# Optimization experiments

Hardware: AMD Instinct MI355X
Metric: run time of the kernel (lower is better)

## Reference

```python
import jax, jax.numpy as jnp
import numpy as np

INPUT_DIM = 1024
HIDDEN_DIM = 1024
BATCH = 8
SEQ = 2048


def setup_inputs() -> dict:
    key = jax.random.key(0)
    ks = jax.random.split(key, 7)
    s = 1.0 / np.sqrt(INPUT_DIM)
    return {
        "subgraph_embeddings": jax.random.normal(ks[0], (BATCH, SEQ, INPUT_DIM), dtype=jnp.float32),
        "Wq": jax.random.uniform(ks[1], (INPUT_DIM, HIDDEN_DIM), jnp.float32, -s, s),
        "bq": jax.random.uniform(ks[2], (HIDDEN_DIM,), jnp.float32, -s, s),
        "Wk": jax.random.uniform(ks[3], (INPUT_DIM, HIDDEN_DIM), jnp.float32, -s, s),
        "bk": jax.random.uniform(ks[4], (HIDDEN_DIM,), jnp.float32, -s, s),
        "Wv": jax.random.uniform(ks[5], (INPUT_DIM, HIDDEN_DIM), jnp.float32, -s, s),
        "bv": jax.random.uniform(ks[6], (HIDDEN_DIM,), jnp.float32, -s, s),
    }


def reference(subgraph_embeddings, Wq, bq, Wk, bk, Wv, bv):
    x = subgraph_embeddings  # [B, S, D]
    Q = jnp.einsum('bsd,dh->bsh', x, Wq) + bq
    K = jnp.einsum('bsd,dh->bsh', x, Wk) + bk
    V = jnp.einsum('bsd,dh->bsh', x, Wv) + bv
    scale = jnp.sqrt(jnp.float32(HIDDEN_DIM))
    scores = jnp.einsum('bqh,bkh->bqk', Q, K) / scale  # [B, S, S]
    weights = jax.nn.softmax(scores, axis=-1)
    return jnp.einsum('bqk,bkh->bqh', weights, V)
```

## Files before the change

kernel.cpp:

```cpp
#include <hip/hip_runtime.h>
#include <hip/hip_bf16.h>
#include <stdint.h>

typedef unsigned short u16;
typedef unsigned int u32;
typedef __attribute__((ext_vector_type(8))) short bf16x8;
typedef __attribute__((ext_vector_type(4))) float f32x4;

#define S_LEN 2048
#define D_DIM 1024
#define H_DIM 1024
#define BATCH 8
#define M_TOTAL (BATCH * S_LEN)

__device__ __forceinline__ u16 f2b(float f) {
  u32 u = __builtin_bit_cast(u32, f);
  u32 r = (u + 0x7fffu + ((u >> 16) & 1u)) >> 16;
  return (u16)r;
}
__device__ __forceinline__ float b2f(u16 v) {
  u32 u = ((u32)v) << 16;
  return __builtin_bit_cast(float, u);
}

__global__ __launch_bounds__(256) void cast_x_kernel(const float* __restrict__ in,
                                                     u16* __restrict__ out, int n8) {
  int i = blockIdx.x * 256 + threadIdx.x;
  if (i >= n8) return;
  const float4* p = (const float4*)in;
  float4 a = p[2 * i], b = p[2 * i + 1];
  u32 w0 = (u32)f2b(a.x) | ((u32)f2b(a.y) << 16);
  u32 w1 = (u32)f2b(a.z) | ((u32)f2b(a.w) << 16);
  u32 w2 = (u32)f2b(b.x) | ((u32)f2b(b.y) << 16);
  u32 w3 = (u32)f2b(b.z) | ((u32)f2b(b.w) << 16);
  ((uint4*)out)[i] = make_uint4(w0, w1, w2, w3);
}

__global__ __launch_bounds__(256) void wcast_kernel(const float* __restrict__ W,
                                                    u16* __restrict__ Wt) {
  __shared__ float tile[32][33];
  int h0 = blockIdx.x * 32, d0 = blockIdx.y * 32;
  int tx = threadIdx.x & 31, ty = threadIdx.x >> 5;
#pragma unroll
  for (int r = ty; r < 32; r += 8)
    tile[r][tx] = W[(size_t)(d0 + r) * H_DIM + h0 + tx];
  __syncthreads();
#pragma unroll
  for (int r = ty; r < 32; r += 8)
    Wt[(size_t)(h0 + r) * D_DIM + d0 + tx] = f2b(tile[tx][r]);
}

template <int BIAS_MODE, bool OUT_BF16>
__global__ __launch_bounds__(256) void gemm_bt(const u16* __restrict__ A,
                                               const u16* __restrict__ Bt,
                                               void* __restrict__ Cout,
                                               const float* __restrict__ bias,
                                               int M, int N, int K,
                                               long long aBatch, long long bBatch,
                                               long long cBatch) {
  __shared__ __align__(16) u16 As[128 * 64];
  __shared__ __align__(16) u16 Bs[128 * 64];
  const int tid = threadIdx.x;
  const int wave = tid >> 6, lane = tid & 63;
  const int quad = lane >> 4, lr = lane & 15;
  const int wr = (wave >> 1) * 64, wc = (wave & 1) * 64;
  const int row0 = blockIdx.x * 128, col0 = blockIdx.y * 128;
  A += (size_t)blockIdx.z * (size_t)aBatch;
  Bt += (size_t)blockIdx.z * (size_t)bBatch;

  f32x4 acc[4][4] = {};

  auto AsL = (__attribute__((address_space(3))) char*)As;
  auto BsL = (__attribute__((address_space(3))) char*)Bs;
  const char* Ab = (const char*)A;
  const char* Bb = (const char*)Bt;

  for (int k0 = 0; k0 < K; k0 += 64) {
#pragma unroll
    for (int rr = 0; rr < 4; ++rr) {
      int chunk = rr * 256 + tid;
      int row = chunk >> 3;
      int cs = (chunk & 7) ^ (row & 7);
      const void* ga = Ab + (((size_t)(row0 + row) * K + (size_t)k0 + cs * 8) * 2);
      __builtin_amdgcn_global_load_lds(
          (const __attribute__((address_space(1))) void*)ga,
          (__attribute__((address_space(3))) void*)(AsL + chunk * 16), 16, 0, 0);
      const void* gb = Bb + (((size_t)(col0 + row) * K + (size_t)k0 + cs * 8) * 2);
      __builtin_amdgcn_global_load_lds(
          (const __attribute__((address_space(1))) void*)gb,
          (__attribute__((address_space(3))) void*)(BsL + chunk * 16), 16, 0, 0);
    }
    __syncthreads();
#pragma unroll
    for (int ks = 0; ks < 2; ++ks) {
      bf16x8 af[4], bf[4];
#pragma unroll
      for (int i = 0; i < 4; ++i) {
        int r = wr + i * 16 + lr;
        int cc = (ks * 4 + quad) ^ (r & 7);
        af[i] = *(const bf16x8*)&As[r * 64 + cc * 8];
      }
#pragma unroll
      for (int j = 0; j < 4; ++j) {
        int r = wc + j * 16 + lr;
        int cc = (ks * 4 + quad) ^ (r & 7);
        bf[j] = *(const bf16x8*)&Bs[r * 64 + cc * 8];
      }
#pragma unroll
      for (int i = 0; i < 4; ++i)
#pragma unroll
        for (int j = 0; j < 4; ++j)
          acc[i][j] = __builtin_amdgcn_mfma_f32_16x16x32_bf16(af[i], bf[j],
                                                              acc[i][j], 0, 0, 0);
    }
    __syncthreads();
  }

  if constexpr (OUT_BF16) {
    u16* C = (u16*)Cout + (size_t)blockIdx.z * (size_t)cBatch;
#pragma unroll
    for (int i = 0; i < 4; ++i) {
#pragma unroll
      for (int j = 0; j < 4; ++j) {
        int c = col0 + wc + j * 16 + lr;
        float bcol = (BIAS_MODE == 1) ? bias[c] : 0.f;
#pragma unroll
        for (int ii = 0; ii < 4; ++ii) {
          int r = row0 + wr + i * 16 + quad * 4 + ii;
          float v = acc[i][j][ii] + bcol;
          if (BIAS_MODE == 2) v += bias[r];
          C[(size_t)r * N + c] = f2b(v);
        }
      }
    }
  } else {
    float* C = (float*)Cout + (size_t)blockIdx.z * (size_t)cBatch;
#pragma unroll
    for (int i = 0; i < 4; ++i) {
#pragma unroll
      for (int j = 0; j < 4; ++j) {
        int c = col0 + wc + j * 16 + lr;
        float bcol = (BIAS_MODE == 1) ? bias[c] : 0.f;
#pragma unroll
        for (int ii = 0; ii < 4; ++ii) {
          int r = row0 + wr + i * 16 + quad * 4 + ii;
          float v = acc[i][j][ii] + bcol;
          if (BIAS_MODE == 2) v += bias[r];
          C[(size_t)r * N + c] = v;
        }
      }
    }
  }
}

__global__ __launch_bounds__(256) void softmax_kernel(u16* __restrict__ S, float scale) {
  __shared__ float red[8];
  const int row = blockIdx.x;
  const int tid = threadIdx.x;
  const int wave = tid >> 6, lane = tid & 63;
  u16* rp = S + (size_t)row * S_LEN;
  uint4 q = ((const uint4*)rp)[tid];
  u32 w[4] = {q.x, q.y, q.z, q.w};
  float v[8];
#pragma unroll
  for (int k = 0; k < 4; ++k) {
    v[2 * k] = b2f((u16)(w[k] & 0xffffu)) * scale;
    v[2 * k + 1] = b2f((u16)(w[k] >> 16)) * scale;
  }
  float m = v[0];
#pragma unroll
  for (int k = 1; k < 8; ++k) m = fmaxf(m, v[k]);
#pragma unroll
  for (int off = 32; off > 0; off >>= 1) m = fmaxf(m, __shfl_xor(m, off));
  if (lane == 0) red[wave] = m;
  __syncthreads();
  m = fmaxf(fmaxf(red[0], red[1]), fmaxf(red[2], red[3]));
  float e[8], s = 0.f;
#pragma unroll
  for (int k = 0; k < 8; ++k) {
    e[k] = __expf(v[k] - m);
    s += e[k];
  }
#pragma unroll
  for (int off = 32; off > 0; off >>= 1) s += __shfl_xor(s, off);
  if (lane == 0) red[4 + wave] = s;
  __syncthreads();
  float inv = 1.0f / (red[4] + red[5] + red[6] + red[7]);
  u32 o[4];
#pragma unroll
  for (int k = 0; k < 4; ++k)
    o[k] = (u32)f2b(e[2 * k] * inv) | ((u32)f2b(e[2 * k + 1] * inv) << 16);
  ((uint4*)rp)[tid] = make_uint4(o[0], o[1], o[2], o[3]);
}

extern "C" void kernel_launch(void* const* d_in, const int* in_sizes, int n_in,
                              void* d_out, int out_size, void* d_ws, size_t ws_size,
                              hipStream_t stream) {
  const float* x = (const float*)d_in[0];
  const float* Wq = (const float*)d_in[1];
  const float* bq = (const float*)d_in[2];
  const float* Wk = (const float*)d_in[3];
  const float* bk = (const float*)d_in[4];
  const float* Wv = (const float*)d_in[5];
  const float* bv = (const float*)d_in[6];
  float* out = (float*)d_out;

  char* ws = (char*)d_ws;
  u16* xb = (u16*)ws;  ws += (size_t)M_TOTAL * D_DIM * 2;
  u16* Wtq = (u16*)ws; ws += (size_t)H_DIM * D_DIM * 2;
  u16* Wtk = (u16*)ws; ws += (size_t)H_DIM * D_DIM * 2;
  u16* Wtv = (u16*)ws; ws += (size_t)H_DIM * D_DIM * 2;
  u16* Qm = (u16*)ws;  ws += (size_t)M_TOTAL * H_DIM * 2;
  u16* Km = (u16*)ws;  ws += (size_t)M_TOTAL * H_DIM * 2;
  u16* Vt = (u16*)ws;  ws += (size_t)BATCH * H_DIM * S_LEN * 2;
  u16* Sm = (u16*)ws;  ws += (size_t)BATCH * S_LEN * S_LEN * 2;

  cast_x_kernel<<<(M_TOTAL * D_DIM / 8 + 255) / 256, 256, 0, stream>>>(
      x, xb, M_TOTAL * D_DIM / 8);
  wcast_kernel<<<dim3(32, 32), 256, 0, stream>>>(Wq, Wtq);
  wcast_kernel<<<dim3(32, 32), 256, 0, stream>>>(Wk, Wtk);
  wcast_kernel<<<dim3(32, 32), 256, 0, stream>>>(Wv, Wtv);

  gemm_bt<1, true><<<dim3(128, 8, 1), 256, 0, stream>>>(
      xb, Wtq, Qm, bq, M_TOTAL, H_DIM, D_DIM, 0, 0, 0);
  gemm_bt<1, true><<<dim3(128, 8, 1), 256, 0, stream>>>(
      xb, Wtk, Km, bk, M_TOTAL, H_DIM, D_DIM, 0, 0, 0);

  gemm_bt<2, true><<<dim3(8, 16, BATCH), 256, 0, stream>>>(
      Wtv, xb, Vt, bv, H_DIM, S_LEN, D_DIM,
      0LL, (long long)S_LEN * D_DIM, (long long)H_DIM * S_LEN);

  gemm_bt<0, true><<<dim3(16, 16, BATCH), 256, 0, stream>>>(
      Qm, Km, Sm, nullptr, S_LEN, S_LEN, H_DIM,
      (long long)S_LEN * H_DIM, (long long)S_LEN * H_DIM, (long long)S_LEN * S_LEN);

  softmax_kernel<<<M_TOTAL, 256, 0, stream>>>(Sm, 0.03125f);

  gemm_bt<0, false><<<dim3(16, 8, BATCH), 256, 0, stream>>>(
      Sm, Vt, out, nullptr, S_LEN, H_DIM, S_LEN,
      (long long)S_LEN * S_LEN, (long long)H_DIM * S_LEN, (long long)S_LEN * H_DIM);
}
```

Measured before the change: 451.6 us.

## Fuse softmax into GEMM epilogues, merge QK projection, use 32x32 MFMA

Replaces the standalone softmax with an exp epilogue in the QK^T GEMM that also accumulates row sums via atomics, and applies the reciprocal sum in the PV GEMM epilogue. Q and K projections are merged into one GEMM over concatenated weights. The three weight casts and bias/lsum setup are combined into one kernel. All GEMMs switch from 16x16x32 to 32x32x16 MFMA. This removes a full read/write pass over the score matrix and several launches, but drops max-subtraction in softmax, risking overflow for large scores, and adds atomic contention.

Result: slower. 477.1 us (+5.7%).

```diff
diff --git a/kernel.cpp b/kernel.cpp
--- a/kernel.cpp
+++ b/kernel.cpp
@@ -5,7 +5,7 @@
 typedef unsigned short u16;
 typedef unsigned int u32;
 typedef __attribute__((ext_vector_type(8))) short bf16x8;
-typedef __attribute__((ext_vector_type(4))) float f32x4;
+typedef __attribute__((ext_vector_type(16))) float f32x16;
 
 #define S_LEN 2048
 #define D_DIM 1024
@@ -36,39 +36,52 @@
   ((uint4*)out)[i] = make_uint4(w0, w1, w2, w3);
 }
 
-__global__ __launch_bounds__(256) void wcast_kernel(const float* __restrict__ W,
-                                                    u16* __restrict__ Wt) {
+__global__ __launch_bounds__(256) void wcast_all_kernel(
+    const float* __restrict__ Wq, const float* __restrict__ Wk,
+    const float* __restrict__ Wv, const float* __restrict__ bq,
+    const float* __restrict__ bk, u16* __restrict__ Wtqk,
+    u16* __restrict__ Wtv, float* __restrict__ bqk, float* __restrict__ lsum) {
   __shared__ float tile[32][33];
+  int z = blockIdx.z;
+  const float* W = (z == 0) ? Wq : (z == 1) ? Wk : Wv;
+  u16* Wt = (z == 0) ? Wtqk : (z == 1) ? (Wtqk + 1024 * 1024) : Wtv;
   int h0 = blockIdx.x * 32, d0 = blockIdx.y * 32;
   int tx = threadIdx.x & 31, ty = threadIdx.x >> 5;
 #pragma unroll
   for (int r = ty; r < 32; r += 8)
     tile[r][tx] = W[(size_t)(d0 + r) * H_DIM + h0 + tx];
+  if (blockIdx.x == 0 && blockIdx.y == 0) {
+    if (z == 0) {
+      for (int i = threadIdx.x; i < 1024; i += 256) bqk[i] = bq[i];
+    } else if (z == 1) {
+      for (int i = threadIdx.x; i < 1024; i += 256) bqk[1024 + i] = bk[i];
+    } else {
+      for (int i = threadIdx.x; i < M_TOTAL; i += 256) lsum[i] = 0.f;
+    }
+  }
   __syncthreads();
 #pragma unroll
   for (int r = ty; r < 32; r += 8)
     Wt[(size_t)(h0 + r) * D_DIM + d0 + tx] = f2b(tile[tx][r]);
 }
 
-template <int BIAS_MODE, bool OUT_BF16>
-__global__ __launch_bounds__(256) void gemm_bt(const u16* __restrict__ A,
-                                               const u16* __restrict__ Bt,
-                                               void* __restrict__ Cout,
-                                               const float* __restrict__ bias,
-                                               int M, int N, int K,
-                                               long long aBatch, long long bBatch,
-                                               long long cBatch) {
+template <int BIAS, int EPI, bool OUT_BF16>
+__global__ __launch_bounds__(256) void gemm32(
+    const u16* __restrict__ A, const u16* __restrict__ Bt, void* __restrict__ Cout,
+    const float* __restrict__ bias, float* __restrict__ lsum,
+    int M, int N, int K, int lda, int ldb, int ldc,
+    long long aBatch, long long bBatch, long long cBatch, float scale) {
   __shared__ __align__(16) u16 As[128 * 64];
   __shared__ __align__(16) u16 Bs[128 * 64];
   const int tid = threadIdx.x;
   const int wave = tid >> 6, lane = tid & 63;
-  const int quad = lane >> 4, lr = lane & 15;
+  const int hlf = lane >> 5, ln = lane & 31;
   const int wr = (wave >> 1) * 64, wc = (wave & 1) * 64;
   const int row0 = blockIdx.x * 128, col0 = blockIdx.y * 128;
   A += (size_t)blockIdx.z * (size_t)aBatch;
   Bt += (size_t)blockIdx.z * (size_t)bBatch;
 
-  f32x4 acc[4][4] = {};
+  f32x16 acc[2][2] = {};
 
   auto AsL = (__attribute__((address_space(3))) char*)As;
   auto BsL = (__attribute__((address_space(3))) char*)Bs;
@@ -81,116 +94,88 @@
       int chunk = rr * 256 + tid;
       int row = chunk >> 3;
       int cs = (chunk & 7) ^ (row & 7);
-      const void* ga = Ab + (((size_t)(row0 + row) * K + (size_t)k0 + cs * 8) * 2);
+      const void* ga = Ab + (((size_t)(row0 + row) * lda + (size_t)k0 + cs * 8) * 2);
       __builtin_amdgcn_global_load_lds(
           (const __attribute__((address_space(1))) void*)ga,
           (__attribute__((address_space(3))) void*)(AsL + chunk * 16), 16, 0, 0);
-      const void* gb = Bb + (((size_t)(col0 + row) * K + (size_t)k0 + cs * 8) * 2);
+      const void* gb = Bb + (((size_t)(col0 + row) * ldb + (size_t)k0 + cs * 8) * 2);
       __builtin_amdgcn_global_load_lds(
           (const __attribute__((address_space(1))) void*)gb,
           (__attribute__((address_space(3))) void*)(BsL + chunk * 16), 16, 0, 0);
     }
     __syncthreads();
 #pragma unroll
-    for (int ks = 0; ks < 2; ++ks) {
-      bf16x8 af[4], bf[4];
-#pragma unroll
-      for (int i = 0; i < 4; ++i) {
-        int r = wr + i * 16 + lr;
-        int cc = (ks * 4 + quad) ^ (r & 7);
-        af[i] = *(const bf16x8*)&As[r * 64 + cc * 8];
+    for (int ks = 0; ks < 4; ++ks) {
+      int c = ks * 2 + hlf;
+      int cc = (c ^ (ln & 7)) * 8;
+      bf16x8 af[2], bf[2];
+#pragma unroll
+      for (int t = 0; t < 2; ++t) {
+        af[t] = *(const bf16x8*)&As[(wr + t * 32 + ln) * 64 + cc];
+        bf[t] = *(const bf16x8*)&Bs[(wc + t * 32 + ln) * 64 + cc];
       }
 #pragma unroll
-      for (int j = 0; j < 4; ++j) {
-        int r = wc + j * 16 + lr;
-        int cc = (ks * 4 + quad) ^ (r & 7);
-        bf[j] = *(const bf16x8*)&Bs[r * 64 + cc * 8];
+      for (int i = 0; i < 2; ++i)
+#pragma unroll
+        for (int j = 0; j < 2; ++j)
+          acc[i][j] = __builtin_amdgcn_mfma_f32_32x32x16_bf16(af[i], bf[j],
+                                                              acc[i][j], 0, 0, 0);
+    }
+    __syncthreads();
+  }
+
+  const long long lrow0 = (long long)blockIdx.z * M + row0;
+
+  if constexpr (EPI == 1) {
+    u16* C = (u16*)Cout + (size_t)blockIdx.z * (size_t)cBatch;
+#pragma unroll
+    for (int i = 0; i < 2; ++i)
+#pragma unroll
+      for (int j = 0; j < 2; ++j)
+#pragma unroll
+        for (int r = 0; r < 16; ++r) {
+          float e = __expf(acc[i][j][r] * scale);
+          acc[i][j][r] = e;
+          int lr_ = wr + i * 32 + (r & 3) + 8 * (r >> 2) + 4 * hlf;
+          int lc_ = wc + j * 32 + ln;
+          C[(size_t)(row0 + lr_) * ldc + (col0 + lc_)] = f2b(e);
+        }
+#pragma unroll
+    for (int i = 0; i < 2; ++i)
+#pragma unroll
+      for (int r = 0; r < 16; ++r) {
+        float v = acc[i][0][r] + acc[i][1][r];
+#pragma unroll
+        for (int off = 1; off < 32; off <<= 1) v += __shfl_xor(v, off);
+        if (ln == 0)
+          atomicAdd(lsum + lrow0 + wr + i * 32 + (r & 3) + 8 * (r >> 2) + 4 * hlf, v);
       }
-#pragma unroll
-      for (int i = 0; i < 4; ++i)
-#pragma unroll
-        for (int j = 0; j < 4; ++j)
-          acc[i][j] = __builtin_amdgcn_mfma_f32_16x16x32_bf16(af[i], bf[j],
-                                                              acc[i][j], 0, 0, 0);
-    }
-    __syncthreads();
-  }
-
-  if constexpr (OUT_BF16) {
-    u16* C = (u16*)Cout + (size_t)blockIdx.z * (size_t)cBatch;
-#pragma unroll
-    for (int i = 0; i < 4; ++i) {
-#pragma unroll
-      for (int j = 0; j < 4; ++j) {
-        int c = col0 + wc + j * 16 + lr;
-        float bcol = (BIAS_MODE == 1) ? bias[c] : 0.f;
-#pragma unroll
-        for (int ii = 0; ii < 4; ++ii) {
-          int r = row0 + wr + i * 16 + quad * 4 + ii;
-          float v = acc[i][j][ii] + bcol;
-          if (BIAS_MODE == 2) v += bias[r];
-          C[(size_t)r * N + c] = f2b(v);
+    return;
+  }
+
+#pragma unroll
+  for (int i = 0; i < 2; ++i) {
+#pragma unroll
+    for (int r = 0; r < 16; ++r) {
+      int lr_ = wr + i * 32 + (r & 3) + 8 * (r >> 2) + 4 * hlf;
+      float radd = 0.f, rmul = 1.f;
+      if (BIAS == 2) radd = bias[row0 + lr_];
+      if (EPI == 2) rmul = 1.0f / lsum[lrow0 + lr_];
+#pragma unroll
+      for (int j = 0; j < 2; ++j) {
+        int lc_ = wc + j * 32 + ln;
+        float v = acc[i][j][r] * rmul + radd;
+        if (BIAS == 1) v += bias[col0 + lc_];
+        if constexpr (OUT_BF16) {
+          u16* C = (u16*)Cout + (size_t)blockIdx.z * (size_t)cBatch;
+          C[(size_t)(row0 + lr_) * ldc + (col0 + lc_)] = f2b(v);
+        } else {
+          float* C = (float*)Cout + (size_t)blockIdx.z * (size_t)cBatch;
+          C[(size_t)(row0 + lr_) * ldc + (col0 + lc_)] = v;
         }
       }
     }
-  } else {
-    float* C = (float*)Cout + (size_t)blockIdx.z * (size_t)cBatch;
-#pragma unroll
-    for (int i = 0; i < 4; ++i) {
-#pragma unroll
-      for (int j = 0; j < 4; ++j) {
-        int c = col0 + wc + j * 16 + lr;
-        float bcol = (BIAS_MODE == 1) ? bias[c] : 0.f;
-#pragma unroll
-        for (int ii = 0; ii < 4; ++ii) {
-          int r = row0 + wr + i * 16 + quad * 4 + ii;
-          float v = acc[i][j][ii] + bcol;
-          if (BIAS_MODE == 2) v += bias[r];
-          C[(size_t)r * N + c] = v;
-        }
-      }
-    }
-  }
-}
-
-__global__ __launch_bounds__(256) void softmax_kernel(u16* __restrict__ S, float scale) {
-  __shared__ float red[8];
-  const int row = blockIdx.x;
-  const int tid = threadIdx.x;
-  const int wave = tid >> 6, lane = tid & 63;
-  u16* rp = S + (size_t)row * S_LEN;
-  uint4 q = ((const uint4*)rp)[tid];
-  u32 w[4] = {q.x, q.y, q.z, q.w};
-  float v[8];
-#pragma unroll
-  for (int k = 0; k < 4; ++k) {
-    v[2 * k] = b2f((u16)(w[k] & 0xffffu)) * scale;
-    v[2 * k + 1] = b2f((u16)(w[k] >> 16)) * scale;
-  }
-  float m = v[0];
-#pragma unroll
-  for (int k = 1; k < 8; ++k) m = fmaxf(m, v[k]);
-#pragma unroll
-  for (int off = 32; off > 0; off >>= 1) m = fmaxf(m, __shfl_xor(m, off));
-  if (lane == 0) red[wave] = m;
-  __syncthreads();
-  m = fmaxf(fmaxf(red[0], red[1]), fmaxf(red[2], red[3]));
-  float e[8], s = 0.f;
-#pragma unroll
-  for (int k = 0; k < 8; ++k) {
-    e[k] = __expf(v[k] - m);
-    s += e[k];
-  }
-#pragma unroll
-  for (int off = 32; off > 0; off >>= 1) s += __shfl_xor(s, off);
-  if (lane == 0) red[4 + wave] = s;
-  __syncthreads();
-  float inv = 1.0f / (red[4] + red[5] + red[6] + red[7]);
-  u32 o[4];
-#pragma unroll
-  for (int k = 0; k < 4; ++k)
-    o[k] = (u32)f2b(e[2 * k] * inv) | ((u32)f2b(e[2 * k + 1] * inv) << 16);
-  ((uint4*)rp)[tid] = make_uint4(o[0], o[1], o[2], o[3]);
+  }
 }
 
 extern "C" void kernel_launch(void* const* d_in, const int* in_sizes, int n_in,
@@ -206,37 +191,38 @@
   float* out = (float*)d_out;
 
   char* ws = (char*)d_ws;
-  u16* xb = (u16*)ws;  ws += (size_t)M_TOTAL * D_DIM * 2;
-  u16* Wtq = (u16*)ws; ws += (size_t)H_DIM * D_DIM * 2;
-  u16* Wtk = (u16*)ws; ws += (size_t)H_DIM * D_DIM * 2;
-  u16* Wtv = (u16*)ws; ws += (size_t)H_DIM * D_DIM * 2;
-  u16* Qm = (u16*)ws;  ws += (size_t)M_TOTAL * H_DIM * 2;
-  u16* Km = (u16*)ws;  ws += (size_t)M_TOTAL * H_DIM * 2;
-  u16* Vt = (u16*)ws;  ws += (size_t)BATCH * H_DIM * S_LEN * 2;
-  u16* Sm = (u16*)ws;  ws += (size_t)BATCH * S_LEN * S_LEN * 2;
+  u16* xb = (u16*)ws;   ws += (size_t)M_TOTAL * D_DIM * 2;
+  u16* Wtqk = (u16*)ws; ws += (size_t)2 * H_DIM * D_DIM * 2;
+  u16* Wtv = (u16*)ws;  ws += (size_t)H_DIM * D_DIM * 2;
+  u16* QKm = (u16*)ws;  ws += (size_t)M_TOTAL * 2 * H_DIM * 2;
+  u16* Vt = (u16*)ws;   ws += (size_t)BATCH * H_DIM * S_LEN * 2;
+  u16* Sm = (u16*)ws;   ws += (size_t)BATCH * S_LEN * S_LEN * 2;
+  float* bqk = (float*)ws;  ws += 2048 * 4;
+  float* lsum = (float*)ws; ws += (size_t)M_TOTAL * 4;
 
   cast_x_kernel<<<(M_TOTAL * D_DIM / 8 + 255) / 256, 256, 0, stream>>>(
       x, xb, M_TOTAL * D_DIM / 8);
-  wcast_kernel<<<dim3(32, 32), 256, 0, stream>>>(Wq, Wtq);
-  wcast_kernel<<<dim3(32, 32), 256, 0, stream>>>(Wk, Wtk);
-  wcast_kernel<<<dim3(32, 32), 256, 0, stream>>>(Wv, Wtv);
-
-  gemm_bt<1, true><<<dim3(128, 8, 1), 256, 0, stream>>>(
-      xb, Wtq, Qm, bq, M_TOTAL, H_DIM, D_DIM, 0, 0, 0);
-  gemm_bt<1, true><<<dim3(128, 8, 1), 256, 0, stream>>>(
-      xb, Wtk, Km, bk, M_TOTAL, H_DIM, D_DIM, 0, 0, 0);
-
-  gemm_bt<2, true><<<dim3(8, 16, BATCH), 256, 0, stream>>>(
-      Wtv, xb, Vt, bv, H_DIM, S_LEN, D_DIM,
-      0LL, (long long)S_LEN * D_DIM, (long long)H_DIM * S_LEN);
-
-  gemm_bt<0, true><<<dim3(16, 16, BATCH), 256, 0, stream>>>(
-      Qm, Km, Sm, nullptr, S_LEN, S_LEN, H_DIM,
-      (long long)S_LEN * H_DIM, (long long)S_LEN * H_DIM, (long long)S_LEN * S_LEN);
-
-  softmax_kernel<<<M_TOTAL, 256, 0, stream>>>(Sm, 0.03125f);
-
-  gemm_bt<0, false><<<dim3(16, 8, BATCH), 256, 0, stream>>>(
-      Sm, Vt, out, nullptr, S_LEN, H_DIM, S_LEN,
-      (long long)S_LEN * S_LEN, (long long)H_DIM * S_LEN, (long long)S_LEN * H_DIM);
-}
+  wcast_all_kernel<<<dim3(32, 32, 3), 256, 0, stream>>>(
+      Wq, Wk, Wv, bq, bk, Wtqk, Wtv, bqk, lsum);
+
+  gemm32<1, 0, true><<<dim3(128, 16, 1), 256, 0, stream>>>(
+      xb, Wtqk, QKm, bqk, nullptr, M_TOTAL, 2 * H_DIM, D_DIM,
+      D_DIM, D_DIM, 2 * H_DIM, 0, 0, 0, 0.f);
+
+  gemm32<2, 0, true><<<dim3(8, 16, BATCH), 256, 0, stream>>>(
+      Wtv, xb, Vt, bv, nullptr, H_DIM, S_LEN, D_DIM,
+      D_DIM, D_DIM, S_LEN,
+      0LL, (long long)S_LEN * D_DIM, (long long)H_DIM * S_LEN, 0.f);
+
+  gemm32<0, 1, true><<<dim3(16, 16, BATCH), 256, 0, stream>>>(
+      QKm, QKm + H_DIM, Sm, nullptr, lsum, S_LEN, S_LEN, H_DIM,
+      2 * H_DIM, 2 * H_DIM, S_LEN,
+      (long long)S_LEN * 2 * H_DIM, (long long)S_LEN * 2 * H_DIM,
+      (long long)S_LEN * S_LEN, 0.03125f);
+
+  gemm32<0, 2, false><<<dim3(16, 8, BATCH), 256, 0, stream>>>(
+      Sm, Vt, out, nullptr, lsum, S_LEN, H_DIM, S_LEN,
+      S_LEN, S_LEN, H_DIM,
+      (long long)S_LEN * S_LEN, (long long)H_DIM * S_LEN,
+      (long long)S_LEN * H_DIM, 0.f);
+}
```
